# Optimization experiments

Hardware: AMD Instinct MI355X
Metric: run time of the kernel (lower is better)

Reference implementation:

```python
import jax, jax.numpy as jnp
import numpy as np

N_NODES = 50000
N_EDGES = 800000
HIDDEN = 64
OUT = 16
N_LAYERS = 3


def setup_inputs() -> dict:
    key = jax.random.key(0)
    ks = jax.random.split(key, 8)
    s = 1.0 / np.sqrt(HIDDEN)
    x = jax.random.normal(ks[0], (N_NODES, HIDDEN), dtype=jnp.float32)
    edge_index = jax.random.randint(ks[1], (2, N_EDGES), 0, N_NODES, dtype=jnp.int64)
    # SAGEConv params per layer: lin_l (neighbor path, with bias), lin_r (root path, no bias)
    Wl = jax.random.uniform(ks[2], (N_LAYERS, HIDDEN, HIDDEN), jnp.float32, -s, s)
    bl = jax.random.uniform(ks[3], (N_LAYERS, HIDDEN), jnp.float32, -s, s)
    Wr = jax.random.uniform(ks[4], (N_LAYERS, HIDDEN, HIDDEN), jnp.float32, -s, s)
    W_out = jax.random.uniform(ks[5], (HIDDEN, OUT), jnp.float32, -s, s)
    b_out = jax.random.uniform(ks[6], (OUT,), jnp.float32, -s, s)
    return {"x": x, "edge_index": edge_index, "Wl": Wl, "bl": bl, "Wr": Wr,
            "W_out": W_out, "b_out": b_out}


def reference(x, edge_index, Wl, bl, Wr, W_out, b_out):
    n = x.shape[0]
    src, dst = edge_index[0], edge_index[1]
    # in-degree for mean aggregation (clamped to 1 to avoid div-by-zero)
    deg = jax.ops.segment_sum(jnp.ones((src.shape[0],), x.dtype), dst, num_segments=n)
    deg = jnp.maximum(deg, 1.0)[:, None]  # [N, 1]
    for l in range(N_LAYERS):
        msg = x[src]                                            # [E, H] gather
        agg = jax.ops.segment_sum(msg, dst, num_segments=n) / deg  # scatter-mean [N, H]
        # SAGEConv: lin_l(agg) + lin_r(x)  (lin_r has no bias)
        x = agg @ Wl[l] + bl[l] + x @ Wr[l]
        x = jax.nn.relu(x)
    return x @ W_out + b_out
```

## Files before the change

### kernel.cpp

```cpp
#include <hip/hip_runtime.h>
#include <hip/hip_bf16.h>

#define NN 50000
#define NE 800000
#define HD 64
#define OD 16
#define CAP 64
#define TILES 3125
#define AST 72
#define SCATB 2048
#define PSZ 6250

typedef unsigned short u16;
typedef unsigned int u32;
typedef __attribute__((ext_vector_type(8))) short short8;
typedef __attribute__((ext_vector_type(4))) float f32x4;

__device__ __forceinline__ float bf2f(u16 v) { return __uint_as_float(((u32)v) << 16); }
__device__ __forceinline__ u16 f2bf(float f) {
  __hip_bfloat16 h = __float2bfloat16(f);
  return *reinterpret_cast<u16*>(&h);
}
__device__ __forceinline__ float ldf(const void* p, long i, bool f32m) {
  return f32m ? ((const float*)p)[i] : bf2f(((const u16*)p)[i]);
}
__device__ __forceinline__ int edge_at(const void* eidx, long pos, bool i64) {
  return i64 ? (int)((const long long*)eidx)[pos] : ((const int*)eidx)[pos];
}

__device__ __forceinline__ bool detect_i64(const u32* e32, int lane) {
  return __ballot(e32[2 * lane + 1] != 0u) == 0ull;
}
__device__ __forceinline__ bool detect_f32(const u32* x32, int lane) {
  u32 v = x32[lane] & 0xffffu;
  int e = (int)((v >> 7) & 0xff);
  bool wild = (v != 0u) && (e < 100 || e > 140);
  return __popcll(__ballot(wild)) > 16;
}

__global__ __launch_bounds__(256) void k_pre(
    const void* __restrict__ x, const void* __restrict__ eidx,
    const void* __restrict__ Wl, const void* __restrict__ bl,
    const void* __restrict__ Wr, const void* __restrict__ Wo,
    const void* __restrict__ bo,
    int* __restrict__ deg, u16* __restrict__ csr, u32* __restrict__ spill,
    u16* __restrict__ xA, u16* __restrict__ wfrag, u16* __restrict__ pfrag,
    float* __restrict__ blf, float* __restrict__ bof,
    int* __restrict__ flags) {
  int lane = threadIdx.x & 63;
  if (blockIdx.x < SCATB) {
    bool i64 = detect_i64((const u32*)eidx, lane);
    int g = blockIdx.x & 7;
    int lo = g * PSZ, hi = lo + PSZ;
    int base = (blockIdx.x >> 3) * 256 + threadIdx.x;
    for (int e = base; e < NE; e += 65536) {
      int dst = edge_at(eidx, (long)NE + e, i64);
      if (dst >= lo && dst < hi) {
        int src = edge_at(eidx, e, i64);
        int pos = atomicAdd(&deg[dst], 1);
        if (pos < CAP) csr[(long)dst * CAP + pos] = (u16)src;
        else {
          int sp = atomicAdd(&flags[4], 1);
          spill[sp] = (u32)dst * 50000u + (u32)src;
        }
      }
    }
  } else {
    bool f32m = detect_f32((const u32*)x, lane);
    int i = (blockIdx.x - SCATB) * 256 + threadIdx.x;
    if (f32m) {
      float4 v = ((const float4*)x)[i];
      u32 lo = (u32)f2bf(v.x) | ((u32)f2bf(v.y) << 16);
      u32 hi = (u32)f2bf(v.z) | ((u32)f2bf(v.w) << 16);
      ((u32*)xA)[2 * i] = lo;
      ((u32*)xA)[2 * i + 1] = hi;
    }
    if (i < 3 * 16 * 64 * 8) {
      int j = i & 7, ln = (i >> 3) & 63, f = (i >> 9) & 15, l = i >> 13;
      int s = f >> 2, c = f & 3;
      int k = 32 * s + ((ln >> 4) << 3) + j;
      int n = (c << 4) + (ln & 15);
      long wbase = (long)l * HD * HD;
      float v = (k < HD) ? ldf(Wl, wbase + (long)k * HD + n, f32m)
                         : ldf(Wr, wbase + (long)(k - HD) * HD + n, f32m);
      wfrag[i] = f2bf(v);
    }
    if (i < 2 * 64 * 8) {
      int j = i & 7, ln = (i >> 3) & 63, s = i >> 9;
      int k = 32 * s + ((ln >> 4) << 3) + j;
      pfrag[i] = f2bf(ldf(Wo, (long)k * OD + (ln & 15), f32m));
    }
    if (i < 3 * HD) blf[i] = ldf(bl, i, f32m);
    if (i < OD) bof[i] = ldf(bo, i, f32m);
  }
}

__global__ __launch_bounds__(256, 8) void k_fused(
    const u16* __restrict__ xin_bf, const u16* __restrict__ xin_f32m,
    const u32* __restrict__ xorig32, u16* __restrict__ xout,
    const int* __restrict__ deg, const u16* __restrict__ csr,
    const u32* __restrict__ spill,
    const u16* __restrict__ wfrag, const u16* __restrict__ pfrag,
    const float* __restrict__ bl3, const float* __restrict__ bof,
    void* __restrict__ outp, int layer, int doProj,
    const int* __restrict__ flags) {
  __shared__ __align__(16) u16 aw[16 * AST];
  __shared__ float sbl[HD];
  __shared__ float sbo[OD];
  if (threadIdx.x < HD) sbl[threadIdx.x] = bl3[layer * HD + threadIdx.x];
  if (threadIdx.x < OD) sbo[threadIdx.x] = bof[threadIdx.x];
  int lane = threadIdx.x & 63;
  bool f32m = detect_f32(xorig32, lane);
  int spillcnt = __builtin_amdgcn_readfirstlane(flags[4]);
  const u16* xin = f32m ? xin_f32m : xin_bf;
  const u32* x32 = (const u32*)xin;

  int w = threadIdx.x >> 6;
  int nb = blockIdx.x * 16;
  int fl = lane & 31;
  int half = lane >> 5;
  u32* aw32 = (u32*)aw;
  int n0 = nb + 4 * w;

  int4 dv = *(const int4*)(deg + n0);
  int dt[4] = {__builtin_amdgcn_readfirstlane(dv.x),
               __builtin_amdgcn_readfirstlane(dv.y),
               __builtin_amdgcn_readfirstlane(dv.z),
               __builtin_amdgcn_readfirstlane(dv.w)};
  int idx[4];
#pragma unroll
  for (int g = 0; g < 4; ++g) {
    int d = dt[g] < CAP ? dt[g] : CAP;
    idx[g] = (lane < d) ? (int)csr[(long)(n0 + g) * CAP + lane] : 0;
  }

  for (int g = 0; g < 4; ++g) {
    int dtot = dt[g];
    int d = dtot < CAP ? dtot : CAP;
    float ax0 = 0.f, ay0 = 0.f, ax1 = 0.f, ay1 = 0.f;
    for (int j = 0; j < d; j += 16) {
      u32 v[8];
#pragma unroll
      for (int p = 0; p < 8; ++p) {
        int se = __builtin_amdgcn_readlane(idx[g], j + 2 * p);
        int so = __builtin_amdgcn_readlane(idx[g], j + 2 * p + 1);
        int s = half ? so : se;
        v[p] = x32[(long)s * 32 + fl];
      }
#pragma unroll
      for (int p = 0; p < 8; ++p) {
        int m = j + 2 * p + half;
        u32 vv = (m < d) ? v[p] : 0u;
        float vlo = __uint_as_float(vv << 16);
        float vhi = __uint_as_float(vv & 0xffff0000u);
        if (p & 1) { ax1 += vlo; ay1 += vhi; }
        else       { ax0 += vlo; ay0 += vhi; }
      }
    }
    float ax = ax0 + ax1, ay = ay0 + ay1;
    ax += __shfl_xor(ax, 32);
    ay += __shfl_xor(ay, 32);
    if (spillcnt > 0) {
      int n = n0 + g;
      for (int base = 0; base < spillcnt; base += 64) {
        u32 p = (base + lane < spillcnt) ? spill[base + lane] : 0xffffffffu;
        u32 dd = p / 50000u;
        u32 ss = p - dd * 50000u;
        unsigned long long mk = __ballot(dd == (u32)n);
        while (mk) {
          int j = __builtin_ctzll(mk);
          mk &= mk - 1;
          int s = __builtin_amdgcn_readlane((int)ss, j);
          u32 v = x32[(long)s * 32 + fl];
          ax += __uint_as_float(v << 16);
          ay += __uint_as_float(v & 0xffff0000u);
        }
      }
    }
    float rd = 1.0f / (float)(dtot > 0 ? dtot : 1);
    if (half == 0)
      aw32[(4 * w + g) * (AST / 2) + fl] =
          (u32)f2bf(ax * rd) | ((u32)f2bf(ay * rd) << 16);
  }
  __syncthreads();

  int quad = lane >> 4, m16 = lane & 15;
  short8 a0 = *(const short8*)(aw + m16 * AST + quad * 8);
  short8 a1 = *(const short8*)(aw + m16 * AST + 32 + quad * 8);
  const u16* xrow = xin + (long)(nb + m16) * HD;
  short8 x2 = *(const short8*)(xrow + quad * 8);
  short8 x3 = *(const short8*)(xrow + 32 + quad * 8);
  int c = w;
  const short8* bp = (const short8*)(wfrag + (long)layer * 16 * 64 * 8);
  short8 b0 = bp[(0 * 4 + c) * 64 + lane];
  short8 b1 = bp[(1 * 4 + c) * 64 + lane];
  short8 b2 = bp[(2 * 4 + c) * 64 + lane];
  short8 b3 = bp[(3 * 4 + c) * 64 + lane];
  float bb = sbl[c * 16 + m16];
  f32x4 acc = (f32x4){bb, bb, bb, bb};
  acc = __builtin_amdgcn_mfma_f32_16x16x32_bf16(a0, b0, acc, 0, 0, 0);
  acc = __builtin_amdgcn_mfma_f32_16x16x32_bf16(a1, b1, acc, 0, 0, 0);
  acc = __builtin_amdgcn_mfma_f32_16x16x32_bf16(x2, b2, acc, 0, 0, 0);
  acc = __builtin_amdgcn_mfma_f32_16x16x32_bf16(x3, b3, acc, 0, 0, 0);
  __syncthreads();

#pragma unroll
  for (int r = 0; r < 4; ++r)
    aw[(quad * 4 + r) * AST + c * 16 + m16] = f2bf(fmaxf(acc[r], 0.f));
  __syncthreads();

  if (!doProj) {
    int row = threadIdx.x >> 4, ch = threadIdx.x & 15;
    uint2 v = *(const uint2*)(aw + row * AST + ch * 4);
    *(uint2*)(xout + (long)(nb + row) * HD + ch * 4) = v;
  } else if (w == 0) {
    short8 pa0 = *(const short8*)(aw + m16 * AST + quad * 8);
    short8 pa1 = *(const short8*)(aw + m16 * AST + 32 + quad * 8);
    const short8* pb = (const short8*)pfrag;
    short8 pb0 = pb[lane];
    short8 pb1 = pb[64 + lane];
    float bv = sbo[m16];
    f32x4 pacc = (f32x4){bv, bv, bv, bv};
    pacc = __builtin_amdgcn_mfma_f32_16x16x32_bf16(pa0, pb0, pacc, 0, 0, 0);
    pacc = __builtin_amdgcn_mfma_f32_16x16x32_bf16(pa1, pb1, pacc, 0, 0, 0);
    if (f32m) {
      float* o = (float*)outp;
#pragma unroll
      for (int r = 0; r < 4; ++r)
        o[(long)(nb + quad * 4 + r) * OD + m16] = pacc[r];
    } else {
      u16* o = (u16*)outp;
#pragma unroll
      for (int r = 0; r < 4; ++r)
        o[(long)(nb + quad * 4 + r) * OD + m16] = f2bf(pacc[r]);
    }
  }
}

extern "C" void kernel_launch(void* const* d_in, const int* in_sizes, int n_in,
                              void* d_out, int out_size, void* d_ws, size_t ws_size,
                              hipStream_t stream) {
  const void* x = d_in[0];
  const void* eidx = d_in[1];
  const void* Wl = d_in[2];
  const void* bl = d_in[3];
  const void* Wr = d_in[4];
  const void* Wo = d_in[5];
  const void* bo = d_in[6];

  char* w = (char*)d_ws;
  size_t off = 0;
  int* flags = (int*)(w + off);     off += 256;
  int* deg = (int*)(w + off);       off += (size_t)NN * 4 + 192;
  size_t memset_bytes = off;
  u16* csr = (u16*)(w + off);       off += (size_t)NN * CAP * 2;
  u32* spill = (u32*)(w + off);     off += (size_t)NE * 4;
  u16* wfrag = (u16*)(w + off);     off += 3 * 16 * 64 * 8 * 2;
  u16* pfrag = (u16*)(w + off);     off += 2 * 64 * 8 * 2;
  float* blf = (float*)(w + off);   off += 3 * HD * 4;
  float* bof = (float*)(w + off);   off += 256;
  u16* xA = (u16*)(w + off);        off += (size_t)NN * HD * 2;
  u16* xB = (u16*)(w + off);        off += (size_t)NN * HD * 2;

  hipMemsetAsync(flags, 0, memset_bytes, stream);

  k_pre<<<SCATB + 3125, 256, 0, stream>>>(x, eidx, Wl, bl, Wr, Wo, bo,
                                          deg, csr, spill, xA, wfrag, pfrag,
                                          blf, bof, flags);

  const u32* xo32 = (const u32*)x;
  k_fused<<<TILES, 256, 0, stream>>>((const u16*)x, xA, xo32, xB, deg, csr, spill,
                                     wfrag, pfrag, blf, bof, (void*)0, 0, 0, flags);
  k_fused<<<TILES, 256, 0, stream>>>(xB, xB, xo32, xA, deg, csr, spill,
                                     wfrag, pfrag, blf, bof, (void*)0, 1, 0, flags);
  k_fused<<<TILES, 256, 0, stream>>>(xA, xA, xo32, (u16*)0, deg, csr, spill,
                                     wfrag, pfrag, blf, bof, d_out, 2, 1, flags);
}
```

Before: 187.2 us.

## Restructure neighbor gather to 16-lane row slices processing two nodes concurrently

```diff
diff --git a/kernel.cpp b/kernel.cpp
--- a/kernel.cpp
+++ b/kernel.cpp
@@ -117,10 +117,10 @@
 
   int w = threadIdx.x >> 6;
   int nb = blockIdx.x * 16;
-  int fl = lane & 31;
-  int half = lane >> 5;
+  int n0 = nb + 4 * w;
+  int grp = lane >> 4;
+  int f = lane & 15;
   u32* aw32 = (u32*)aw;
-  int n0 = nb + 4 * w;
 
   int4 dv = *(const int4*)(deg + n0);
   int dt[4] = {__builtin_amdgcn_readfirstlane(dv.x),
@@ -134,53 +134,70 @@
     idx[g] = (lane < d) ? (int)csr[(long)(n0 + g) * CAP + lane] : 0;
   }
 
-  for (int g = 0; g < 4; ++g) {
-    int dtot = dt[g];
-    int d = dtot < CAP ? dtot : CAP;
-    float ax0 = 0.f, ay0 = 0.f, ax1 = 0.f, ay1 = 0.f;
-    for (int j = 0; j < d; j += 16) {
-      u32 v[8];
-#pragma unroll
-      for (int p = 0; p < 8; ++p) {
-        int se = __builtin_amdgcn_readlane(idx[g], j + 2 * p);
-        int so = __builtin_amdgcn_readlane(idx[g], j + 2 * p + 1);
-        int s = half ? so : se;
-        v[p] = x32[(long)s * 32 + fl];
-      }
-#pragma unroll
-      for (int p = 0; p < 8; ++p) {
-        int m = j + 2 * p + half;
-        u32 vv = (m < d) ? v[p] : 0u;
-        float vlo = __uint_as_float(vv << 16);
-        float vhi = __uint_as_float(vv & 0xffff0000u);
-        if (p & 1) { ax1 += vlo; ay1 += vhi; }
-        else       { ax0 += vlo; ay0 += vhi; }
-      }
-    }
-    float ax = ax0 + ax1, ay = ay0 + ay1;
-    ax += __shfl_xor(ax, 32);
-    ay += __shfl_xor(ay, 32);
-    if (spillcnt > 0) {
-      int n = n0 + g;
-      for (int base = 0; base < spillcnt; base += 64) {
-        u32 p = (base + lane < spillcnt) ? spill[base + lane] : 0xffffffffu;
-        u32 dd = p / 50000u;
-        u32 ss = p - dd * 50000u;
-        unsigned long long mk = __ballot(dd == (u32)n);
-        while (mk) {
-          int j = __builtin_ctzll(mk);
-          mk &= mk - 1;
-          int s = __builtin_amdgcn_readlane((int)ss, j);
-          u32 v = x32[(long)s * 32 + fl];
-          ax += __uint_as_float(v << 16);
-          ay += __uint_as_float(v & 0xffff0000u);
-        }
-      }
-    }
-    float rd = 1.0f / (float)(dtot > 0 ? dtot : 1);
-    if (half == 0)
-      aw32[(4 * w + g) * (AST / 2) + fl] =
-          (u32)f2bf(ax * rd) | ((u32)f2bf(ay * rd) << 16);
+#pragma unroll
+  for (int ph = 0; ph < 2; ++ph) {
+    const u32* xph = x32 + ph * 16;
+#pragma unroll
+    for (int gp = 0; gp < 4; gp += 2) {
+      int dA = dt[gp] < CAP ? dt[gp] : CAP;
+      int dB = dt[gp + 1] < CAP ? dt[gp + 1] : CAP;
+      int dmax = dA > dB ? dA : dB;
+      float alo = 0.f, ahi = 0.f, blo = 0.f, bhi = 0.f;
+      for (int j = 0; j < dmax; j += 16) {
+        u32 va[4], vb[4];
+#pragma unroll
+        for (int p = 0; p < 4; ++p) {
+          int sa = __shfl(idx[gp], j + 4 * p + grp);
+          int sb = __shfl(idx[gp + 1], j + 4 * p + grp);
+          va[p] = xph[(long)sa * 32 + f];
+          vb[p] = xph[(long)sb * 32 + f];
+        }
+#pragma unroll
+        for (int p = 0; p < 4; ++p) {
+          int m = j + 4 * p + grp;
+          u32 a = (m < dA) ? va[p] : 0u;
+          u32 b = (m < dB) ? vb[p] : 0u;
+          alo += __uint_as_float(a << 16);
+          ahi += __uint_as_float(a & 0xffff0000u);
+          blo += __uint_as_float(b << 16);
+          bhi += __uint_as_float(b & 0xffff0000u);
+        }
+      }
+      alo += __shfl_xor(alo, 16); ahi += __shfl_xor(ahi, 16);
+      blo += __shfl_xor(blo, 16); bhi += __shfl_xor(bhi, 16);
+      alo += __shfl_xor(alo, 32); ahi += __shfl_xor(ahi, 32);
+      blo += __shfl_xor(blo, 32); bhi += __shfl_xor(bhi, 32);
+      if (spillcnt > 0) {
+#pragma unroll
+        for (int q = 0; q < 2; ++q) {
+          int n = n0 + gp + q;
+          for (int base = 0; base < spillcnt; base += 64) {
+            u32 p = (base + lane < spillcnt) ? spill[base + lane] : 0xffffffffu;
+            u32 dd = p / 50000u;
+            u32 ss = p - dd * 50000u;
+            unsigned long long mk = __ballot(dd == (u32)n);
+            while (mk) {
+              int jj = __builtin_ctzll(mk);
+              mk &= mk - 1;
+              int s = __builtin_amdgcn_readlane((int)ss, jj);
+              u32 v = xph[(long)s * 32 + f];
+              float vlo = __uint_as_float(v << 16);
+              float vhi = __uint_as_float(v & 0xffff0000u);
+              if (q) { blo += vlo; bhi += vhi; }
+              else   { alo += vlo; ahi += vhi; }
+            }
+          }
+        }
+      }
+      if (lane < 16) {
+        float rdA = 1.0f / (float)(dt[gp] > 0 ? dt[gp] : 1);
+        float rdB = 1.0f / (float)(dt[gp + 1] > 0 ? dt[gp + 1] : 1);
+        aw32[(4 * w + gp) * (AST / 2) + ph * 16 + f] =
+            (u32)f2bf(alo * rdA) | ((u32)f2bf(ahi * rdA) << 16);
+        aw32[(4 * w + gp + 1) * (AST / 2) + ph * 16 + f] =
+            (u32)f2bf(blo * rdB) | ((u32)f2bf(bhi * rdB) << 16);
+      }
+    }
   }
   __syncthreads();
 
```

New measurement: 190.0 us. About the same (+1.5%).

## Gather neighbor rows with 128-bit loads and interleave four nodes per wave

Applied to the files above, without the earlier changes.

```diff
diff --git a/kernel.cpp b/kernel.cpp
--- a/kernel.cpp
+++ b/kernel.cpp
@@ -15,6 +15,7 @@
 typedef unsigned int u32;
 typedef __attribute__((ext_vector_type(8))) short short8;
 typedef __attribute__((ext_vector_type(4))) float f32x4;
+typedef __attribute__((ext_vector_type(4))) unsigned int u32x4;
 
 __device__ __forceinline__ float bf2f(u16 v) { return __uint_as_float(((u32)v) << 16); }
 __device__ __forceinline__ u16 f2bf(float f) {
@@ -95,7 +96,7 @@
   }
 }
 
-__global__ __launch_bounds__(256, 8) void k_fused(
+__global__ __launch_bounds__(256, 6) void k_fused(
     const u16* __restrict__ xin_bf, const u16* __restrict__ xin_f32m,
     const u32* __restrict__ xorig32, u16* __restrict__ xout,
     const int* __restrict__ deg, const u16* __restrict__ csr,
@@ -113,54 +114,62 @@
   bool f32m = detect_f32(xorig32, lane);
   int spillcnt = __builtin_amdgcn_readfirstlane(flags[4]);
   const u16* xin = f32m ? xin_f32m : xin_bf;
-  const u32* x32 = (const u32*)xin;
+  const u32x4* x128 = (const u32x4*)xin;
 
   int w = threadIdx.x >> 6;
   int nb = blockIdx.x * 16;
-  int fl = lane & 31;
-  int half = lane >> 5;
+  int n0 = nb + 4 * w;
+  int grp = lane >> 3;
+  int f = lane & 7;
   u32* aw32 = (u32*)aw;
-  int n0 = nb + 4 * w;
 
   int4 dv = *(const int4*)(deg + n0);
   int dt[4] = {__builtin_amdgcn_readfirstlane(dv.x),
                __builtin_amdgcn_readfirstlane(dv.y),
                __builtin_amdgcn_readfirstlane(dv.z),
                __builtin_amdgcn_readfirstlane(dv.w)};
+  int d[4], dmax = 0;
   int idx[4];
 #pragma unroll
   for (int g = 0; g < 4; ++g) {
-    int d = dt[g] < CAP ? dt[g] : CAP;
-    idx[g] = (lane < d) ? (int)csr[(long)(n0 + g) * CAP + lane] : 0;
-  }
-
-  for (int g = 0; g < 4; ++g) {
-    int dtot = dt[g];
-    int d = dtot < CAP ? dtot : CAP;
-    float ax0 = 0.f, ay0 = 0.f, ax1 = 0.f, ay1 = 0.f;
-    for (int j = 0; j < d; j += 16) {
-      u32 v[8];
-#pragma unroll
-      for (int p = 0; p < 8; ++p) {
-        int se = __builtin_amdgcn_readlane(idx[g], j + 2 * p);
-        int so = __builtin_amdgcn_readlane(idx[g], j + 2 * p + 1);
-        int s = half ? so : se;
-        v[p] = x32[(long)s * 32 + fl];
+    d[g] = dt[g] < CAP ? dt[g] : CAP;
+    if (d[g] > dmax) dmax = d[g];
+    idx[g] = (lane < d[g]) ? (int)csr[(long)(n0 + g) * CAP + lane] : 0;
+  }
+
+  float lo[4][4] = {}, hi[4][4] = {};
+  for (int j = 0; j < dmax; j += 8) {
+    u32x4 v[4];
+#pragma unroll
+    for (int g = 0; g < 4; ++g) {
+      int s = __shfl(idx[g], j + grp);
+      v[g] = x128[(long)s * 8 + f];
+    }
+#pragma unroll
+    for (int g = 0; g < 4; ++g) {
+      bool ok = (j + grp) < d[g];
+#pragma unroll
+      for (int q = 0; q < 4; ++q) {
+        u32 vv = ok ? v[g][q] : 0u;
+        lo[g][q] += __uint_as_float(vv << 16);
+        hi[g][q] += __uint_as_float(vv & 0xffff0000u);
       }
-#pragma unroll
-      for (int p = 0; p < 8; ++p) {
-        int m = j + 2 * p + half;
-        u32 vv = (m < d) ? v[p] : 0u;
-        float vlo = __uint_as_float(vv << 16);
-        float vhi = __uint_as_float(vv & 0xffff0000u);
-        if (p & 1) { ax1 += vlo; ay1 += vhi; }
-        else       { ax0 += vlo; ay0 += vhi; }
-      }
-    }
-    float ax = ax0 + ax1, ay = ay0 + ay1;
-    ax += __shfl_xor(ax, 32);
-    ay += __shfl_xor(ay, 32);
-    if (spillcnt > 0) {
+    }
+  }
+#pragma unroll
+  for (int g = 0; g < 4; ++g)
+#pragma unroll
+    for (int q = 0; q < 4; ++q) {
+      lo[g][q] += __shfl_xor(lo[g][q], 8);
+      hi[g][q] += __shfl_xor(hi[g][q], 8);
+      lo[g][q] += __shfl_xor(lo[g][q], 16);
+      hi[g][q] += __shfl_xor(hi[g][q], 16);
+      lo[g][q] += __shfl_xor(lo[g][q], 32);
+      hi[g][q] += __shfl_xor(hi[g][q], 32);
+    }
+  if (spillcnt > 0) {
+#pragma unroll
+    for (int g = 0; g < 4; ++g) {
       int n = n0 + g;
       for (int base = 0; base < spillcnt; base += 64) {
         u32 p = (base + lane < spillcnt) ? spill[base + lane] : 0xffffffffu;
@@ -168,19 +177,28 @@
         u32 ss = p - dd * 50000u;
         unsigned long long mk = __ballot(dd == (u32)n);
         while (mk) {
-          int j = __builtin_ctzll(mk);
+          int jj = __builtin_ctzll(mk);
           mk &= mk - 1;
-          int s = __builtin_amdgcn_readlane((int)ss, j);
-          u32 v = x32[(long)s * 32 + fl];
-          ax += __uint_as_float(v << 16);
-          ay += __uint_as_float(v & 0xffff0000u);
+          int s = __builtin_amdgcn_readlane((int)ss, jj);
+          u32x4 v = x128[(long)s * 8 + f];
+#pragma unroll
+          for (int q = 0; q < 4; ++q) {
+            lo[g][q] += __uint_as_float(v[q] << 16);
+            hi[g][q] += __uint_as_float(v[q] & 0xffff0000u);
+          }
         }
       }
     }
-    float rd = 1.0f / (float)(dtot > 0 ? dtot : 1);
-    if (half == 0)
-      aw32[(4 * w + g) * (AST / 2) + fl] =
-          (u32)f2bf(ax * rd) | ((u32)f2bf(ay * rd) << 16);
+  }
+  if (lane < 8) {
+#pragma unroll
+    for (int g = 0; g < 4; ++g) {
+      float rd = 1.0f / (float)(dt[g] > 0 ? dt[g] : 1);
+      int rb = (4 * w + g) * (AST / 2) + 4 * f;
+#pragma unroll
+      for (int q = 0; q < 4; ++q)
+        aw32[rb + q] = (u32)f2bf(lo[g][q] * rd) | ((u32)f2bf(hi[g][q] * rd) << 16);
+    }
   }
   __syncthreads();
 
@@ -269,7 +287,8 @@
                                           blf, bof, flags);
 
   const u32* xo32 = (const u32*)x;
-  k_fused<<<TILES, 256, 0, stream>>>((const u16*)x, xA, xo32, xB, deg, csr, spill,
+  const u16* x16 = (const u16*)x;
+  k_fused<<<TILES, 256, 0, stream>>>(x16, xA, xo32, xB, deg, csr, spill,
                                      wfrag, pfrag, blf, bof, (void*)0, 0, 0, flags);
   k_fused<<<TILES, 256, 0, stream>>>(xB, xB, xo32, xA, deg, csr, spill,
                                      wfrag, pfrag, blf, bof, (void*)0, 1, 0, flags);
```

Measured after the change: 191.0 us. +2.0%, slower.
